# Kernel tuning notes

Hardware: AMD Instinct MI355X
Metric: run time of the kernel (lower is better)

The kernel has to match this reference:

```python
import jax, jax.numpy as jnp
import numpy as np

NUM_TOKENS = 50265  # roberta-base vocab size
CONTEXT_LEN = 384
BS = 4
N_DATASET = 2048


def setup_inputs() -> dict:
    key = jax.random.key(0)
    k1, k2, k3 = jax.random.split(key, 3)
    dataset_tokens = jax.random.randint(k1, (N_DATASET, CONTEXT_LEN), 0, NUM_TOKENS)
    input_tokens = jax.random.randint(k2, (BS, CONTEXT_LEN), 0, NUM_TOKENS)
    # t in (0,1): avoid exact endpoints where log((1-t)/T) -> -inf
    t = jax.random.uniform(k3, (BS,), minval=0.05, maxval=0.95, dtype=jnp.float32)
    return {"input_tokens": input_tokens, "dataset_tokens": dataset_tokens, "t": t}


def reference(input_tokens, dataset_tokens, t):
    """EmpiricalDFM.calculate_uniform_probabilities, dataset given as one array.

    flow[b,c,s] = sum_n exp(logp[n,b]) * onehot(dataset_tokens)[n,c,s] / sum_n exp(logp[n,b])
               = sum_n softmax_n(logp[:,b]) * onehot(dataset_tokens)[n,c,s]
    The original torch code computes exactly this via an online (streamed)
    log-sum-exp accumulation over dataset batches; softmax over the full
    dataset axis is the mathematically identical single-pass form.
    """
    bs, c = input_tokens.shape
    n = dataset_tokens.shape[0]
    T = NUM_TOKENS

    # (n, bs): number of positions where dataset row matches input row
    match_count = (dataset_tokens[:, None, :] == input_tokens[None, :, :]).sum(-1).astype(t.dtype)

    log_a = jnp.log(t + (1.0 - t) / T)          # (bs,) prob of match per position
    log_b = jnp.log((1.0 - t) / T)              # (bs,) prob of mismatch per position
    logp = match_count * log_a[None, :] + (c - match_count) * log_b[None, :]  # (n, bs)

    # Normalized weights over the dataset axis (stable log-sum-exp built in).
    w = jax.nn.softmax(logp, axis=0)            # (n, bs)

    # Weighted one-hot accumulate WITHOUT materializing the (n,c,V) one-hot:
    # flow[b, pos, dataset_tokens[j, pos]] += w[j, b]
    c_idx = jnp.broadcast_to(jnp.arange(c)[None, :], (n, c))
    flow = jnp.zeros((bs, c, T), dtype=t.dtype)
    flow = flow.at[:, c_idx, dataset_tokens].add(w.T[:, :, None])  # scatter over (bs, n, c)
    return flow
```

## Files before the change

### kernel.cpp

```cpp
#include <hip/hip_runtime.h>

constexpr int T_VOCAB = 50265;
constexpr int CLEN    = 384;
constexpr int BSZ     = 4;
constexpr int NDATA   = 2048;
constexpr int NPT     = NDATA / 256;
constexpr int CHUNK   = 6720;
constexpr int SLICES  = 8;
constexpr int SCOLS   = CLEN / SLICES;

typedef float f32x4 __attribute__((ext_vector_type(4)));

__global__ __launch_bounds__(256) void k_transpose(
    const int* __restrict__ ds, int* __restrict__ dsT)
{
    __shared__ int tile[64][65];
    const int n0 = blockIdx.x * 64;
    const int s0 = blockIdx.y * 64;
    const int lane = threadIdx.x & 63;
    const int quad = threadIdx.x >> 6;
    #pragma unroll
    for (int k = 0; k < 16; ++k) {
        const int r = quad + 4 * k;
        tile[r][lane] = ds[(size_t)(n0 + r) * CLEN + s0 + lane];
    }
    __syncthreads();
    #pragma unroll
    for (int k = 0; k < 16; ++k) {
        const int c = quad + 4 * k;
        dsT[(size_t)(s0 + c) * NDATA + n0 + lane] = tile[lane][c];
    }
}

__global__ __launch_bounds__(256) void k_match(
    const int* __restrict__ dsT,
    const int* __restrict__ in_tok,
    int* __restrict__ pcount)
{
    const int nt = blockIdx.x & 7;
    const int sl = blockIdx.x >> 3;
    const int n  = nt * 256 + threadIdx.x;
    const int sbase = sl * SCOLS;
    int c0 = 0, c1 = 0, c2 = 0, c3 = 0;
    #pragma unroll 4
    for (int j = 0; j < SCOLS; ++j) {
        const int s = sbase + j;
        const int tok = dsT[(size_t)s * NDATA + n];
        c0 += (tok == in_tok[0 * CLEN + s]);
        c1 += (tok == in_tok[1 * CLEN + s]);
        c2 += (tok == in_tok[2 * CLEN + s]);
        c3 += (tok == in_tok[3 * CLEN + s]);
    }
    pcount[(sl * BSZ + 0) * NDATA + n] = c0;
    pcount[(sl * BSZ + 1) * NDATA + n] = c1;
    pcount[(sl * BSZ + 2) * NDATA + n] = c2;
    pcount[(sl * BSZ + 3) * NDATA + n] = c3;
}

__global__ __launch_bounds__(256) void k_weights(
    const int* __restrict__ pcount,
    const float* __restrict__ t,
    float* __restrict__ w)
{
    const int b = blockIdx.x;
    const int tid = threadIdx.x;
    const float tv = t[b];
    const float la = logf(tv + (1.0f - tv) / (float)T_VOCAB);
    const float lb = logf((1.0f - tv) / (float)T_VOCAB);

    float lp[NPT];
    float m = -INFINITY;
    #pragma unroll
    for (int k = 0; k < NPT; ++k) {
        const int n = tid + k * 256;
        int cnt = 0;
        #pragma unroll
        for (int sl = 0; sl < SLICES; ++sl)
            cnt += pcount[(sl * BSZ + b) * NDATA + n];
        const float mc = (float)cnt;
        lp[k] = mc * la + ((float)CLEN - mc) * lb;
        m = fmaxf(m, lp[k]);
    }
    #pragma unroll
    for (int off = 32; off >= 1; off >>= 1) m = fmaxf(m, __shfl_xor(m, off));
    __shared__ float redm[4], reds[4];
    const int wid = tid >> 6;
    if ((tid & 63) == 0) redm[wid] = m;
    __syncthreads();
    const float M = fmaxf(fmaxf(redm[0], redm[1]), fmaxf(redm[2], redm[3]));

    float e[NPT];
    float sum = 0.0f;
    #pragma unroll
    for (int k = 0; k < NPT; ++k) { e[k] = expf(lp[k] - M); sum += e[k]; }
    #pragma unroll
    for (int off = 32; off >= 1; off >>= 1) sum += __shfl_xor(sum, off);
    if ((tid & 63) == 0) reds[wid] = sum;
    __syncthreads();
    const float inv = 1.0f / (reds[0] + reds[1] + reds[2] + reds[3]);
    #pragma unroll
    for (int k = 0; k < NPT; ++k) w[b * NDATA + tid + k * 256] = e[k] * inv;
}

template <bool USE_T>
__global__ __launch_bounds__(256) void k_scatter(
    const int* __restrict__ ds_tok,
    const int* __restrict__ dsT,
    const float* __restrict__ w,
    float* __restrict__ out)
{
    __shared__ float lds[CHUNK + 4];
    const int tid = threadIdx.x;
    const int bid = blockIdx.x;
    const int b = bid & (BSZ - 1);
    const int s = bid >> 2;

    int   tok[NPT];
    float wv[NPT];
    #pragma unroll
    for (int k = 0; k < NPT; ++k) {
        const int n = tid + k * 256;
        tok[k] = USE_T ? dsT[(size_t)s * NDATA + n]
                       : ds_tok[(size_t)n * CLEN + s];
        wv[k] = w[b * NDATA + n];
    }

    const size_t row_elem0 = ((size_t)b * CLEN + s) * (size_t)T_VOCAB;
    float* rowp = out + row_elem0;
    const int align_off = (int)(row_elem0 & 3);

    for (int c0 = 0; c0 < T_VOCAB; c0 += CHUNK) {
        const int nch = (T_VOCAB - c0 < CHUNK) ? (T_VOCAB - c0) : CHUNK;
        const int tot = nch + align_off;
        f32x4* l4 = (f32x4*)lds;
        const int nz4 = (tot + 3) >> 2;
        for (int i = tid; i < nz4; i += 256) l4[i] = (f32x4){0.f, 0.f, 0.f, 0.f};
        __syncthreads();
        #pragma unroll
        for (int k = 0; k < NPT; ++k) {
            const unsigned off = (unsigned)(tok[k] - c0);
            if (off < (unsigned)nch) atomicAdd(&lds[off + align_off], wv[k]);
        }
        __syncthreads();
        int head = (4 - align_off) & 3;
        if (head > nch) head = nch;
        if (tid < head) rowp[c0 + tid] = lds[tid + align_off];
        const int nv = (nch - head) >> 2;
        const f32x4* l4s = (const f32x4*)lds + (align_off ? 1 : 0);
        f32x4* dst4 = (f32x4*)(rowp + c0 + head);
        for (int i = tid; i < nv; i += 256)
            __builtin_nontemporal_store(l4s[i], &dst4[i]);
        const int ts = head + (nv << 2);
        for (int i = ts + tid; i < nch; i += 256) rowp[c0 + i] = lds[i + align_off];
        __syncthreads();
    }
}

__global__ __launch_bounds__(256) void k_match_logp_fb(
    const int* __restrict__ in_tok, const int* __restrict__ ds_tok,
    const float* __restrict__ t, float* __restrict__ logp)
{
    __shared__ int s_in[BSZ * CLEN];
    __shared__ float s_la[BSZ], s_lb[BSZ];
    const int tid = threadIdx.x;
    for (int i = tid; i < BSZ * CLEN; i += 256) s_in[i] = in_tok[i];
    if (tid < BSZ) {
        float tv = t[tid];
        s_la[tid] = logf(tv + (1.0f - tv) / (float)T_VOCAB);
        s_lb[tid] = logf((1.0f - tv) / (float)T_VOCAB);
    }
    __syncthreads();
    const int n = blockIdx.x * 256 + tid;
    int mc[BSZ] = {0, 0, 0, 0};
    const int4* row = (const int4*)(ds_tok + (size_t)n * CLEN);
    for (int j = 0; j < CLEN / 4; ++j) {
        int4 v = row[j];
        int s = 4 * j;
        #pragma unroll
        for (int b = 0; b < BSZ; ++b)
            mc[b] += (v.x == s_in[b*CLEN+s]) + (v.y == s_in[b*CLEN+s+1]) +
                     (v.z == s_in[b*CLEN+s+2]) + (v.w == s_in[b*CLEN+s+3]);
    }
    #pragma unroll
    for (int b = 0; b < BSZ; ++b) {
        float m = (float)mc[b];
        logp[b * NDATA + n] = m * s_la[b] + ((float)CLEN - m) * s_lb[b];
    }
}

__global__ __launch_bounds__(256) void k_softmax_fb(
    const float* __restrict__ logp, float* __restrict__ w)
{
    const int b = blockIdx.x;
    const int tid = threadIdx.x;
    float lp[NPT];
    float m = -INFINITY;
    #pragma unroll
    for (int k = 0; k < NPT; ++k) {
        lp[k] = logp[b * NDATA + tid + k * 256];
        m = fmaxf(m, lp[k]);
    }
    #pragma unroll
    for (int off = 32; off >= 1; off >>= 1) m = fmaxf(m, __shfl_xor(m, off));
    __shared__ float redm[4], reds[4];
    const int wid = tid >> 6;
    if ((tid & 63) == 0) redm[wid] = m;
    __syncthreads();
    const float M = fmaxf(fmaxf(redm[0], redm[1]), fmaxf(redm[2], redm[3]));
    float e[NPT];
    float sum = 0.0f;
    #pragma unroll
    for (int k = 0; k < NPT; ++k) { e[k] = expf(lp[k] - M); sum += e[k]; }
    #pragma unroll
    for (int off = 32; off >= 1; off >>= 1) sum += __shfl_xor(sum, off);
    if ((tid & 63) == 0) reds[wid] = sum;
    __syncthreads();
    const float inv = 1.0f / (reds[0] + reds[1] + reds[2] + reds[3]);
    #pragma unroll
    for (int k = 0; k < NPT; ++k) w[b * NDATA + tid + k * 256] = e[k] * inv;
}

extern "C" void kernel_launch(void* const* d_in, const int* in_sizes, int n_in,
                              void* d_out, int out_size, void* d_ws, size_t ws_size,
                              hipStream_t stream) {
    const int*   in_tok = (const int*)d_in[0];
    const int*   ds_tok = (const int*)d_in[1];
    const float* t      = (const float*)d_in[2];
    float* out = (float*)d_out;

    int*   dsT    = (int*)d_ws;
    int*   pcount = dsT + (size_t)CLEN * NDATA;
    float* w      = (float*)(pcount + SLICES * BSZ * NDATA);
    float* logp   = w + BSZ * NDATA;

    const size_t need = ((size_t)CLEN * NDATA + (size_t)SLICES * BSZ * NDATA) * sizeof(int)
                      + (size_t)2 * BSZ * NDATA * sizeof(float);

    if (ws_size >= need) {
        k_transpose<<<dim3(NDATA / 64, CLEN / 64), 256, 0, stream>>>(ds_tok, dsT);
        k_match<<<64, 256, 0, stream>>>(dsT, in_tok, pcount);
        k_weights<<<BSZ, 256, 0, stream>>>(pcount, t, w);
        k_scatter<true><<<BSZ * CLEN, 256, 0, stream>>>(ds_tok, dsT, w, out);
    } else {
        k_match_logp_fb<<<NDATA / 256, 256, 0, stream>>>(in_tok, ds_tok, t, logp);
        k_softmax_fb<<<BSZ, 256, 0, stream>>>(logp, w);
        k_scatter<false><<<BSZ * CLEN, 256, 0, stream>>>(ds_tok, dsT, w, out);
    }
}
```

Measured before the change: 344.4 us.

## Fuse transpose with match counting and split scatter across vocab chunks

Merges the transpose and match-count kernels so match counts are computed from the shared-memory tile while transposing, removing one launch and a re-read of the transposed dataset. The scatter kernel now uses a 2D grid with one block per (row, vocab chunk) instead of looping over chunks serially inside each block. This raises parallelism for the output write, which dominates runtime, but each block now reloads its tokens and weights, using vectorized loads. The fallback path reuses the workspace for its logp and weight buffers.

```diff
diff --git a/kernel.cpp b/kernel.cpp
--- a/kernel.cpp
+++ b/kernel.cpp
@@ -6,55 +6,55 @@
 constexpr int NDATA   = 2048;
 constexpr int NPT     = NDATA / 256;
 constexpr int CHUNK   = 6720;
-constexpr int SLICES  = 8;
-constexpr int SCOLS   = CLEN / SLICES;
+constexpr int NCHUNK  = (T_VOCAB + CHUNK - 1) / CHUNK;
+constexpr int SLICES  = CLEN / 64;
 
 typedef float f32x4 __attribute__((ext_vector_type(4)));
 
-__global__ __launch_bounds__(256) void k_transpose(
-    const int* __restrict__ ds, int* __restrict__ dsT)
+__global__ __launch_bounds__(256) void k_transpose_match(
+    const int* __restrict__ ds,
+    const int* __restrict__ in_tok,
+    int* __restrict__ dsT,
+    int* __restrict__ pcount)
 {
     __shared__ int tile[64][65];
-    const int n0 = blockIdx.x * 64;
-    const int s0 = blockIdx.y * 64;
+    __shared__ int s_in[BSZ][64];
+    __shared__ int cnt[64][BSZ];
+    const int n0   = blockIdx.x * 64;
+    const int s0   = blockIdx.y * 64;
     const int lane = threadIdx.x & 63;
     const int quad = threadIdx.x >> 6;
+    {
+        const int b = quad;
+        s_in[b][lane] = in_tok[b * CLEN + s0 + lane];
+        cnt[lane][b]  = 0;
+    }
     #pragma unroll
     for (int k = 0; k < 16; ++k) {
         const int r = quad + 4 * k;
         tile[r][lane] = ds[(size_t)(n0 + r) * CLEN + s0 + lane];
     }
     __syncthreads();
+    int c0 = 0, c1 = 0, c2 = 0, c3 = 0;
     #pragma unroll
     for (int k = 0; k < 16; ++k) {
         const int c = quad + 4 * k;
-        dsT[(size_t)(s0 + c) * NDATA + n0 + lane] = tile[lane][c];
-    }
-}
-
-__global__ __launch_bounds__(256) void k_match(
-    const int* __restrict__ dsT,
-    const int* __restrict__ in_tok,
-    int* __restrict__ pcount)
-{
-    const int nt = blockIdx.x & 7;
-    const int sl = blockIdx.x >> 3;
-    const int n  = nt * 256 + threadIdx.x;
-    const int sbase = sl * SCOLS;
-    int c0 = 0, c1 = 0, c2 = 0, c3 = 0;
-    #pragma unroll 4
-    for (int j = 0; j < SCOLS; ++j) {
-        const int s = sbase + j;
-        const int tok = dsT[(size_t)s * NDATA + n];
-        c0 += (tok == in_tok[0 * CLEN + s]);
-        c1 += (tok == in_tok[1 * CLEN + s]);
-        c2 += (tok == in_tok[2 * CLEN + s]);
-        c3 += (tok == in_tok[3 * CLEN + s]);
-    }
-    pcount[(sl * BSZ + 0) * NDATA + n] = c0;
-    pcount[(sl * BSZ + 1) * NDATA + n] = c1;
-    pcount[(sl * BSZ + 2) * NDATA + n] = c2;
-    pcount[(sl * BSZ + 3) * NDATA + n] = c3;
+        const int tok = tile[lane][c];
+        dsT[(size_t)(s0 + c) * NDATA + n0 + lane] = tok;
+        c0 += (tok == s_in[0][c]);
+        c1 += (tok == s_in[1][c]);
+        c2 += (tok == s_in[2][c]);
+        c3 += (tok == s_in[3][c]);
+    }
+    atomicAdd(&cnt[lane][0], c0);
+    atomicAdd(&cnt[lane][1], c1);
+    atomicAdd(&cnt[lane][2], c2);
+    atomicAdd(&cnt[lane][3], c3);
+    __syncthreads();
+    {
+        const int b = quad;
+        pcount[((size_t)blockIdx.y * BSZ + b) * NDATA + n0 + lane] = cnt[lane][b];
+    }
 }
 
 __global__ __launch_bounds__(256) void k_weights(
@@ -111,49 +111,57 @@
 {
     __shared__ float lds[CHUNK + 4];
     const int tid = threadIdx.x;
-    const int bid = blockIdx.x;
-    const int b = bid & (BSZ - 1);
-    const int s = bid >> 2;
+    const int row = blockIdx.x;
+    const int b = row & (BSZ - 1);
+    const int s = row >> 2;
+    const int c0 = blockIdx.y * CHUNK;
+    const int nch = (T_VOCAB - c0 < CHUNK) ? (T_VOCAB - c0) : CHUNK;
 
     int   tok[NPT];
     float wv[NPT];
-    #pragma unroll
-    for (int k = 0; k < NPT; ++k) {
-        const int n = tid + k * 256;
-        tok[k] = USE_T ? dsT[(size_t)s * NDATA + n]
-                       : ds_tok[(size_t)n * CLEN + s];
-        wv[k] = w[b * NDATA + n];
+    if (USE_T) {
+        const int4*  tp = (const int4*)(dsT + (size_t)s * NDATA) + tid * 2;
+        const f32x4* wp = (const f32x4*)(w + (size_t)b * NDATA) + tid * 2;
+        int4  ta = tp[0], tb = tp[1];
+        f32x4 wa = wp[0], wb = wp[1];
+        tok[0] = ta.x; tok[1] = ta.y; tok[2] = ta.z; tok[3] = ta.w;
+        tok[4] = tb.x; tok[5] = tb.y; tok[6] = tb.z; tok[7] = tb.w;
+        wv[0] = wa.x; wv[1] = wa.y; wv[2] = wa.z; wv[3] = wa.w;
+        wv[4] = wb.x; wv[5] = wb.y; wv[6] = wb.z; wv[7] = wb.w;
+    } else {
+        #pragma unroll
+        for (int k = 0; k < NPT; ++k) {
+            const int n = tid + k * 256;
+            tok[k] = ds_tok[(size_t)n * CLEN + s];
+            wv[k]  = w[(size_t)b * NDATA + n];
+        }
     }
 
     const size_t row_elem0 = ((size_t)b * CLEN + s) * (size_t)T_VOCAB;
     float* rowp = out + row_elem0;
     const int align_off = (int)(row_elem0 & 3);
 
-    for (int c0 = 0; c0 < T_VOCAB; c0 += CHUNK) {
-        const int nch = (T_VOCAB - c0 < CHUNK) ? (T_VOCAB - c0) : CHUNK;
-        const int tot = nch + align_off;
-        f32x4* l4 = (f32x4*)lds;
-        const int nz4 = (tot + 3) >> 2;
-        for (int i = tid; i < nz4; i += 256) l4[i] = (f32x4){0.f, 0.f, 0.f, 0.f};
-        __syncthreads();
-        #pragma unroll
-        for (int k = 0; k < NPT; ++k) {
-            const unsigned off = (unsigned)(tok[k] - c0);
-            if (off < (unsigned)nch) atomicAdd(&lds[off + align_off], wv[k]);
-        }
-        __syncthreads();
-        int head = (4 - align_off) & 3;
-        if (head > nch) head = nch;
-        if (tid < head) rowp[c0 + tid] = lds[tid + align_off];
-        const int nv = (nch - head) >> 2;
-        const f32x4* l4s = (const f32x4*)lds + (align_off ? 1 : 0);
-        f32x4* dst4 = (f32x4*)(rowp + c0 + head);
-        for (int i = tid; i < nv; i += 256)
-            __builtin_nontemporal_store(l4s[i], &dst4[i]);
-        const int ts = head + (nv << 2);
-        for (int i = ts + tid; i < nch; i += 256) rowp[c0 + i] = lds[i + align_off];
-        __syncthreads();
-    }
+    const int tot = nch + align_off;
+    f32x4* l4 = (f32x4*)lds;
+    const int nz4 = (tot + 3) >> 2;
+    for (int i = tid; i < nz4; i += 256) l4[i] = (f32x4){0.f, 0.f, 0.f, 0.f};
+    __syncthreads();
+    #pragma unroll
+    for (int k = 0; k < NPT; ++k) {
+        const unsigned off = (unsigned)(tok[k] - c0);
+        if (off < (unsigned)nch) atomicAdd(&lds[off + align_off], wv[k]);
+    }
+    __syncthreads();
+    int head = (4 - align_off) & 3;
+    if (head > nch) head = nch;
+    if (tid < head) rowp[c0 + tid] = lds[tid + align_off];
+    const int nv = (nch - head) >> 2;
+    const f32x4* l4s = (const f32x4*)lds + (align_off ? 1 : 0);
+    f32x4* dst4 = (f32x4*)(rowp + c0 + head);
+    for (int i = tid; i < nv; i += 256)
+        __builtin_nontemporal_store(l4s[i], &dst4[i]);
+    const int ts = head + (nv << 2);
+    for (int i = ts + tid; i < nch; i += 256) rowp[c0 + i] = lds[i + align_off];
 }
 
 __global__ __launch_bounds__(256) void k_match_logp_fb(
@@ -172,9 +180,9 @@
     __syncthreads();
     const int n = blockIdx.x * 256 + tid;
     int mc[BSZ] = {0, 0, 0, 0};
-    const int4* row = (const int4*)(ds_tok + (size_t)n * CLEN);
+    const int4* rowv = (const int4*)(ds_tok + (size_t)n * CLEN);
     for (int j = 0; j < CLEN / 4; ++j) {
-        int4 v = row[j];
+        int4 v = rowv[j];
         int s = 4 * j;
         #pragma unroll
         for (int b = 0; b < BSZ; ++b)
@@ -231,19 +239,19 @@
     int*   dsT    = (int*)d_ws;
     int*   pcount = dsT + (size_t)CLEN * NDATA;
     float* w      = (float*)(pcount + SLICES * BSZ * NDATA);
-    float* logp   = w + BSZ * NDATA;
 
     const size_t need = ((size_t)CLEN * NDATA + (size_t)SLICES * BSZ * NDATA) * sizeof(int)
-                      + (size_t)2 * BSZ * NDATA * sizeof(float);
+                      + (size_t)BSZ * NDATA * sizeof(float);
 
     if (ws_size >= need) {
-        k_transpose<<<dim3(NDATA / 64, CLEN / 64), 256, 0, stream>>>(ds_tok, dsT);
-        k_match<<<64, 256, 0, stream>>>(dsT, in_tok, pcount);
+        k_transpose_match<<<dim3(NDATA / 64, CLEN / 64), 256, 0, stream>>>(ds_tok, in_tok, dsT, pcount);
         k_weights<<<BSZ, 256, 0, stream>>>(pcount, t, w);
-        k_scatter<true><<<BSZ * CLEN, 256, 0, stream>>>(ds_tok, dsT, w, out);
+        k_scatter<true><<<dim3(BSZ * CLEN, NCHUNK), 256, 0, stream>>>(ds_tok, dsT, w, out);
     } else {
-        k_match_logp_fb<<<NDATA / 256, 256, 0, stream>>>(in_tok, ds_tok, t, logp);
-        k_softmax_fb<<<BSZ, 256, 0, stream>>>(logp, w);
-        k_scatter<false><<<BSZ * CLEN, 256, 0, stream>>>(ds_tok, dsT, w, out);
-    }
-}
+        float* logp_fb = (float*)d_ws;
+        float* w_fb    = logp_fb + BSZ * NDATA;
+        k_match_logp_fb<<<NDATA / 256, 256, 0, stream>>>(in_tok, ds_tok, t, logp_fb);
+        k_softmax_fb<<<BSZ, 256, 0, stream>>>(logp_fb, w_fb);
+        k_scatter<false><<<dim3(BSZ * CLEN, NCHUNK), 256, 0, stream>>>(ds_tok, (const int*)d_ws, w_fb, out);
+    }
+}
```

Result: faster. 335.8 us (-2.5%).
